# Optimization experiments

Hardware: AMD Instinct MI355X
Metric: run time of the kernel (lower is better)

The kernel has to match this reference:

```python
import jax, jax.numpy as jnp
import numpy as np

LAG = 5
MSG_HID = 256
N_ATOMS = 30
N_EDGES = N_ATOMS * (N_ATOMS - 1)  # 870
BATCH = 2
T = 200


def _rel_matrices():
    # fully-connected directed graph, no self loops (standard NRI encoding)
    recv, send = [], []
    for i in range(N_ATOMS):
        for j in range(N_ATOMS):
            if i != j:
                recv.append(i)
                send.append(j)
    rel_rec = np.zeros((N_EDGES, N_ATOMS), dtype=np.float32)
    rel_send = np.zeros((N_EDGES, N_ATOMS), dtype=np.float32)
    rel_rec[np.arange(N_EDGES), recv] = 1.0
    rel_send[np.arange(N_EDGES), send] = 1.0
    return jnp.asarray(rel_rec), jnp.asarray(rel_send)


def setup_inputs() -> dict:
    key = jax.random.key(0)
    ks = jax.random.split(key, 14)
    rel_rec, rel_send = _rel_matrices()
    s = 0.05
    return {
        "inputs": jax.random.normal(ks[0], (BATCH, N_ATOMS, T), jnp.float32),
        "mu": jax.random.normal(ks[1], (BATCH, N_EDGES), jnp.float32),
        "logvar": jax.random.normal(ks[2], (BATCH, N_EDGES), jnp.float32) * 0.1,
        "eps": jax.random.normal(ks[3], (BATCH, N_EDGES), jnp.float32),
        "rel_rec": rel_rec,
        "rel_send": rel_send,
        "w_msg1": jax.random.normal(ks[4], (2 * LAG, MSG_HID), jnp.float32) * s,
        "b_msg1": jnp.zeros((MSG_HID,), jnp.float32),
        "w_msg2": jax.random.normal(ks[5], (MSG_HID, MSG_HID), jnp.float32) * s,
        "b_msg2": jnp.zeros((MSG_HID,), jnp.float32),
        "w_out1": jax.random.normal(ks[6], (LAG + MSG_HID, MSG_HID), jnp.float32) * s,
        "b_out1": jnp.zeros((MSG_HID,), jnp.float32),
        "w_out2": jax.random.normal(ks[7], (MSG_HID, MSG_HID), jnp.float32) * s,
        "b_out2": jnp.zeros((MSG_HID,), jnp.float32),
        "w_out3": jax.random.normal(ks[8], (MSG_HID, 1), jnp.float32) * s,
        "b_out3": jnp.zeros((1,), jnp.float32),
    }


def reference(inputs, mu, logvar, eps, rel_rec, rel_send,
              w_msg1, b_msg1, w_msg2, b_msg2,
              w_out1, b_out1, w_out2, b_out2, w_out3, b_out3):
    # reparametrize: edges [B, E]
    edges = eps * jnp.exp(0.5 * logvar) + mu

    # lag-stack: data [B, T-lag, N, lag]
    Tm = inputs.shape[2] - LAG
    data = jnp.stack([inputs[:, :, i:i + Tm] for i in range(LAG)], axis=-1)
    data = jnp.transpose(data, (0, 2, 1, 3))  # [B, Tm, N, lag]

    # gather node features to edges via one-hot matmuls
    receivers = jnp.einsum('en,btnl->btel', rel_rec, data)   # [B, Tm, E, lag]
    senders = jnp.einsum('en,btnl->btel', rel_send, data)    # [B, Tm, E, lag]
    pre_msg = jnp.concatenate([senders, receivers], axis=-1)  # [B, Tm, E, 2*lag]

    msg = jax.nn.relu(pre_msg @ w_msg1 + b_msg1)
    msg = jax.nn.relu(msg @ w_msg2 + b_msg2)                 # [B, Tm, E, hid]
    msg = msg * edges[:, None, :, None]                       # edge mask

    # scatter-aggregate messages back to receiver nodes
    agg_msgs = jnp.einsum('bteh,en->btnh', msg, rel_rec)      # [B, Tm, N, hid]

    aug = jnp.concatenate([data, agg_msgs], axis=-1)          # [B, Tm, N, lag+hid]
    pred = jax.nn.relu(aug @ w_out1 + b_out1)
    pred = jax.nn.relu(pred @ w_out2 + b_out2)
    pred = (pred @ w_out3 + b_out3)[..., 0]                   # [B, Tm, N]

    return jnp.transpose(pred, (0, 2, 1))                     # [B, N, Tm]
```

## Files before the change

kernel.cpp:

```cpp
#include <hip/hip_runtime.h>

#define LAG 5
#define HID 256
#define NA 30
#define NE 870
#define TM 195
#define TT 200
#define NB 2
#define EPN 29
#define TB3 65
#define NROWS (NB * TM * NA)
#define APAD 4
#define KC 32
#define UVB 1463
#define W2F_ELEMS (HID * HID)
#define W1F_ELEMS (HID * 288)

typedef _Float16 f16;
typedef _Float16 f16x8 __attribute__((ext_vector_type(8)));
typedef float floatx4 __attribute__((ext_vector_type(4)));
typedef float floatx16 __attribute__((ext_vector_type(16)));

__global__ __launch_bounds__(256) void k1_prep(
    const float* __restrict__ inputs, const float* __restrict__ w_msg1,
    const float* __restrict__ b_msg1, const float* __restrict__ w_msg2,
    const float* __restrict__ w_out1, const float* __restrict__ w_out2,
    f16* __restrict__ u, f16* __restrict__ v, f16* __restrict__ w2frag,
    f16* __restrict__ w1frag, f16* __restrict__ w2ofrag)
{
    const int bid = blockIdx.x, tid = threadIdx.x;
    if (bid < UVB) {
        __shared__ float feats8[8][LAG];
        const int r0 = bid * 8;
        if (tid < 8 * LAG) {
            const int i = tid / LAG, l = tid % LAG;
            const int r = r0 + i;
            float fv = 0.f;
            if (r < NROWS) {
                const int b = r / (TM * NA), rem = r % (TM * NA);
                const int t = rem / NA, n = rem % NA;
                fv = inputs[(b * NA + n) * TT + t + l];
            }
            feats8[i][l] = fv;
        }
        float w1c[2 * LAG];
        #pragma unroll
        for (int k = 0; k < 2 * LAG; ++k) w1c[k] = w_msg1[k * HID + tid];
        const float bb = b_msg1[tid];
        __syncthreads();
        #pragma unroll
        for (int i = 0; i < 8; ++i) {
            const int r = r0 + i;
            if (r < NROWS) {
                float ua = bb, va = 0.f;
                #pragma unroll
                for (int l = 0; l < LAG; ++l) {
                    ua = fmaf(feats8[i][l], w1c[l], ua);
                    va = fmaf(feats8[i][l], w1c[LAG + l], va);
                }
                u[(r << 8) + tid] = (f16)ua;
                v[(r << 8) + tid] = (f16)va;
            }
        }
    } else if (bid < UVB + 32) {
        const int fidx = (bid - UVB) * 256 + tid;
        const int lane = fidx & 63;
        const int kc = (fidx >> 6) & 15;
        const int c32 = fidx >> 10;
        const int col = c32 * 32 + (lane & 31);
        const int kb = kc * 16 + (lane >> 5) * 8;
        f16x8 vv;
        #pragma unroll
        for (int x = 0; x < 8; ++x) vv[x] = (f16)w_msg2[(kb + x) * HID + col];
        *(f16x8*)&w2frag[fidx * 8] = vv;
    } else if (bid < UVB + 32 + 36) {
        const int fidx = (bid - (UVB + 32)) * 256 + tid;
        const int lane = fidx & 63;
        const int kc = (fidx >> 6) % 9;
        const int ntc = fidx / (64 * 9);
        const int col = ntc * 16 + (lane & 15);
        const int kb = kc * KC + (lane >> 4) * 8;
        f16x8 vv;
        #pragma unroll
        for (int x = 0; x < 8; ++x) {
            const int k = kb + x;
            float val;
            if (k < 256)      val = w_out1[(5 + k) * HID + col];
            else if (k < 261) val = w_out1[(k - 256) * HID + col];
            else              val = 0.f;
            vv[x] = (f16)val;
        }
        *(f16x8*)&w1frag[fidx * 8] = vv;
    } else {
        const int fidx = (bid - (UVB + 32 + 36)) * 256 + tid;
        const int lane = fidx & 63;
        const int kc = (fidx >> 6) & 7;
        const int ntc = fidx >> 9;
        const int col = ntc * 16 + (lane & 15);
        const int kb = kc * KC + (lane >> 4) * 8;
        f16x8 vv;
        #pragma unroll
        for (int x = 0; x < 8; ++x) vv[x] = (f16)w_out2[(kb + x) * HID + col];
        *(f16x8*)&w2ofrag[fidx * 8] = vv;
    }
}

__global__ __launch_bounds__(256, 3) void k2_msg(
    const f16* __restrict__ u, const f16* __restrict__ v,
    const f16* __restrict__ w2frag,
    const float* __restrict__ mu, const float* __restrict__ logvar,
    const float* __restrict__ eps, const float* __restrict__ b_msg2,
    f16* __restrict__ agg)
{
    __shared__ f16 a_lds[96 * 256];
    __shared__ float ev_lds[32];

    const int bid = blockIdx.x;
    const int n  = bid % NA;
    const int tb = (bid / NA) % TB3;
    const int b  = bid / (NA * TB3);
    const int t0 = tb * 3;
    const int tid = threadIdx.x;
    const int lane = tid & 63, w = tid >> 6;
    const int h = lane >> 5, l31 = lane & 31;

    if (tid < 32) {
        float evv = 0.f;
        if (tid < EPN) {
            const int e = b * NE + n * EPN + tid;
            evv = eps[e] * __expf(0.5f * logvar[e]) + mu[e];
        }
        ev_lds[tid] = evv;
    }

    const f16x8 z8 = {(f16)0, (f16)0, (f16)0, (f16)0, (f16)0, (f16)0, (f16)0, (f16)0};

    const int sbase = (b * TM + t0) * NA;
    #pragma unroll
    for (int i = 0; i < 12; ++i) {
        const int task = i * 256 + tid;
        const int row = task >> 5, c = task & 31;
        const int tt = row >> 5, ei = row & 31;
        f16x8 out8 = z8;
        if (ei < EPN) {
            const int j = ei + (ei >= n);
            const f16x8 uu = *(const f16x8*)(u + (((sbase + tt * NA + j) << 8) + c * 8));
            const f16x8 vv = *(const f16x8*)(v + (((sbase + tt * NA + n) << 8) + c * 8));
            out8 = __builtin_elementwise_max(uu + vv, z8);
        }
        *(f16x8*)&a_lds[row * 256 + ((c * 8) ^ ((row & 7) << 3))] = out8;
    }

    const f16* bbase = w2frag + (lane << 3);
    f16x8 b0[2], b1[2], b2[2];
    #pragma unroll
    for (int nt = 0; nt < 2; ++nt) {
        const int c32 = w * 2 + nt;
        b0[nt] = *(const f16x8*)(bbase + (((c32 * 16) + 0) << 9));
        b1[nt] = *(const f16x8*)(bbase + (((c32 * 16) + 1) << 9));
    }

    floatx16 acc[3][2];
    #pragma unroll
    for (int mt = 0; mt < 3; ++mt)
        #pragma unroll
        for (int nt = 0; nt < 2; ++nt)
            #pragma unroll
            for (int x = 0; x < 16; ++x) acc[mt][nt][x] = 0.f;

    __syncthreads();

    #pragma unroll
    for (int kc = 0; kc < 16; ++kc) {
        if (kc < 14) {
            #pragma unroll
            for (int nt = 0; nt < 2; ++nt)
                b2[nt] = *(const f16x8*)(bbase + ((((w * 2 + nt) * 16) + kc + 2) << 9));
        }
        f16x8 af[3];
        #pragma unroll
        for (int mt = 0; mt < 3; ++mt) {
            const int row = mt * 32 + l31;
            af[mt] = *(const f16x8*)&a_lds[row * 256 + ((kc * 16 + h * 8) ^ ((row & 7) << 3))];
        }
        #pragma unroll
        for (int nt = 0; nt < 2; ++nt)
            #pragma unroll
            for (int mt = 0; mt < 3; ++mt)
                acc[mt][nt] = __builtin_amdgcn_mfma_f32_32x32x16_f16(af[mt], b0[nt], acc[mt][nt], 0, 0, 0);
        #pragma unroll
        for (int nt = 0; nt < 2; ++nt) { b0[nt] = b1[nt]; b1[nt] = b2[nt]; }
    }

    float evr[16];
    #pragma unroll
    for (int reg = 0; reg < 16; ++reg)
        evr[reg] = ev_lds[(reg & 3) + 8 * (reg >> 2) + 4 * h];
    float b2s[2];
    #pragma unroll
    for (int nt = 0; nt < 2; ++nt) b2s[nt] = b_msg2[w * 64 + nt * 32 + l31];

    #pragma unroll
    for (int mt = 0; mt < 3; ++mt) {
        const int t = t0 + mt;
        #pragma unroll
        for (int nt = 0; nt < 2; ++nt) {
            float part = 0.f;
            #pragma unroll
            for (int reg = 0; reg < 16; ++reg)
                part += evr[reg] * fmaxf(acc[mt][nt][reg] + b2s[nt], 0.f);
            part += __shfl_xor(part, 32, 64);
            if (h == 0)
                agg[(((b * TM + t) * NA + n) << 8) + w * 64 + nt * 32 + l31] = (f16)part;
        }
    }
}

__global__ __launch_bounds__(256) void k3_out(
    const f16* __restrict__ agg, const float* __restrict__ inputs,
    const f16* __restrict__ w1frag, const f16* __restrict__ w2ofrag,
    const float* __restrict__ b_out1, const float* __restrict__ b_out2,
    const float* __restrict__ w_out3, const float* __restrict__ b_out3,
    float* __restrict__ out)
{
    __shared__ f16 a1[16][288 + APAD];
    __shared__ float red[4][16];

    const int R0 = blockIdx.x * 16;
    const int tid = threadIdx.x;
    const int lane = tid & 63, w = tid >> 6;
    const int q = lane >> 4, m15 = lane & 15;
    const int wbase = w * 64;

    #pragma unroll
    for (int i = 0; i < 2; ++i) {
        const int task = i * 256 + tid;
        const int row = task >> 5, c = task & 31;
        const int R = R0 + row;
        f16x8 val;
        if (R < NROWS) {
            val = *(const f16x8*)&agg[(R << 8) + c * 8];
        } else {
            for (int x = 0; x < 8; ++x) val[x] = (f16)0.f;
        }
        *(f16x8*)&a1[row][c * 8] = val;
    }
    if (tid < 16) {
        const int R = R0 + tid;
        if (R < NROWS) {
            const int b = R / (TM * NA), rem = R % (TM * NA);
            const int t = rem / NA, n = rem % NA;
            const float* ip = inputs + (b * NA + n) * TT + t;
            #pragma unroll
            for (int l = 0; l < LAG; ++l) a1[tid][256 + l] = (f16)ip[l];
            #pragma unroll
            for (int k = 261; k < 288; ++k) a1[tid][k] = (f16)0.f;
        } else {
            for (int k = 256; k < 288; ++k) a1[tid][k] = (f16)0.f;
        }
    }

    floatx4 acc[4];
    #pragma unroll
    for (int nt = 0; nt < 4; ++nt) acc[nt] = (floatx4){0.f, 0.f, 0.f, 0.f};

    const f16* b1base = w1frag + (lane << 3);
    f16x8 bcur[4], bnxt[4];
    #pragma unroll
    for (int nt = 0; nt < 4; ++nt)
        bcur[nt] = *(const f16x8*)(b1base + (((w * 4 + nt) * 9 + 0) << 9));

    __syncthreads();

    #pragma unroll
    for (int kc = 0; kc < 9; ++kc) {
        if (kc < 8) {
            #pragma unroll
            for (int nt = 0; nt < 4; ++nt)
                bnxt[nt] = *(const f16x8*)(b1base + (((w * 4 + nt) * 9 + kc + 1) << 9));
        }
        const f16x8 af = *(const f16x8*)&a1[m15][kc * KC + q * 8];
        #pragma unroll
        for (int nt = 0; nt < 4; ++nt)
            acc[nt] = __builtin_amdgcn_mfma_f32_16x16x32_f16(af, bcur[nt], acc[nt], 0, 0, 0);
        #pragma unroll
        for (int nt = 0; nt < 4; ++nt) bcur[nt] = bnxt[nt];
    }
    __syncthreads();

    {
        float b1v[4];
        #pragma unroll
        for (int nt = 0; nt < 4; ++nt) b1v[nt] = b_out1[wbase + nt * 16 + m15];
        #pragma unroll
        for (int nt = 0; nt < 4; ++nt)
            #pragma unroll
            for (int reg = 0; reg < 4; ++reg)
                a1[q * 4 + reg][wbase + nt * 16 + m15] =
                    (f16)fmaxf(acc[nt][reg] + b1v[nt], 0.f);
    }

    #pragma unroll
    for (int nt = 0; nt < 4; ++nt) acc[nt] = (floatx4){0.f, 0.f, 0.f, 0.f};

    const f16* b2base = w2ofrag + (lane << 3);
    #pragma unroll
    for (int nt = 0; nt < 4; ++nt)
        bcur[nt] = *(const f16x8*)(b2base + (((w * 4 + nt) * 8 + 0) << 9));

    __syncthreads();

    #pragma unroll
    for (int kc = 0; kc < 8; ++kc) {
        if (kc < 7) {
            #pragma unroll
            for (int nt = 0; nt < 4; ++nt)
                bnxt[nt] = *(const f16x8*)(b2base + (((w * 4 + nt) * 8 + kc + 1) << 9));
        }
        const f16x8 af = *(const f16x8*)&a1[m15][kc * KC + q * 8];
        #pragma unroll
        for (int nt = 0; nt < 4; ++nt)
            acc[nt] = __builtin_amdgcn_mfma_f32_16x16x32_f16(af, bcur[nt], acc[nt], 0, 0, 0);
        #pragma unroll
        for (int nt = 0; nt < 4; ++nt) bcur[nt] = bnxt[nt];
    }

    {
        float b2v[4], w3v[4];
        #pragma unroll
        for (int nt = 0; nt < 4; ++nt) {
            const int col = wbase + nt * 16 + m15;
            b2v[nt] = b_out2[col];
            w3v[nt] = w_out3[col];
        }
        #pragma unroll
        for (int reg = 0; reg < 4; ++reg) {
            float p = 0.f;
            #pragma unroll
            for (int nt = 0; nt < 4; ++nt)
                p += fmaxf(acc[nt][reg] + b2v[nt], 0.f) * w3v[nt];
            p += __shfl_xor(p, 1, 64);
            p += __shfl_xor(p, 2, 64);
            p += __shfl_xor(p, 4, 64);
            p += __shfl_xor(p, 8, 64);
            if (m15 == 0) red[w][q * 4 + reg] = p;
        }
    }
    __syncthreads();
    if (tid < 16) {
        const int R = R0 + tid;
        if (R < NROWS) {
            const float val = red[0][tid] + red[1][tid] + red[2][tid] + red[3][tid] + b_out3[0];
            const int b = R / (TM * NA), rem = R % (TM * NA);
            const int t = rem / NA, n = rem % NA;
            out[(b * NA + n) * TM + t] = val;
        }
    }
}

extern "C" void kernel_launch(void* const* d_in, const int* in_sizes, int n_in,
                              void* d_out, int out_size, void* d_ws, size_t ws_size,
                              hipStream_t stream) {
    const float* inputs  = (const float*)d_in[0];
    const float* mu      = (const float*)d_in[1];
    const float* logvar  = (const float*)d_in[2];
    const float* eps     = (const float*)d_in[3];
    const float* w_msg1  = (const float*)d_in[6];
    const float* b_msg1  = (const float*)d_in[7];
    const float* w_msg2  = (const float*)d_in[8];
    const float* b_msg2  = (const float*)d_in[9];
    const float* w_out1  = (const float*)d_in[10];
    const float* b_out1  = (const float*)d_in[11];
    const float* w_out2  = (const float*)d_in[12];
    const float* b_out2  = (const float*)d_in[13];
    const float* w_out3  = (const float*)d_in[14];
    const float* b_out3  = (const float*)d_in[15];
    float* out = (float*)d_out;

    f16* u       = (f16*)d_ws;
    f16* v       = u       + NROWS * HID;
    f16* aggw    = v       + NROWS * HID;
    f16* w2frag  = aggw    + NROWS * HID;
    f16* w1frag  = w2frag  + W2F_ELEMS;
    f16* w2ofrag = w1frag  + W1F_ELEMS;

    hipLaunchKernelGGL(k1_prep, dim3(UVB + 32 + 36 + 32), dim3(256), 0, stream,
                       inputs, w_msg1, b_msg1, w_msg2, w_out1, w_out2,
                       u, v, w2frag, w1frag, w2ofrag);
    hipLaunchKernelGGL(k2_msg, dim3(NB * NA * TB3), dim3(256), 0, stream,
                       u, v, w2frag, mu, logvar, eps, b_msg2, aggw);
    hipLaunchKernelGGL(k3_out, dim3((NROWS + 15) / 16), dim3(256), 0, stream,
                       aggw, inputs, w1frag, w2ofrag, b_out1, b_out2, w_out3, b_out3, out);
}
```

Measured before the change: 162.8 us.

## Use 8-wave k2 blocks, XCD-aware block remap, and MFMA priority hints

```diff
diff --git a/kernel.cpp b/kernel.cpp
--- a/kernel.cpp
+++ b/kernel.cpp
@@ -15,6 +15,9 @@
 #define UVB 1463
 #define W2F_ELEMS (HID * HID)
 #define W1F_ELEMS (HID * 288)
+#define NWG2 (NB * NA * TB3)
+#define Q8 (NWG2 / 8)
+#define R8 (NWG2 % 8)
 
 typedef _Float16 f16;
 typedef _Float16 f16x8 __attribute__((ext_vector_type(8)));
@@ -105,7 +108,7 @@
     }
 }
 
-__global__ __launch_bounds__(256, 3) void k2_msg(
+__global__ __launch_bounds__(512, 4) void k2_msg(
     const f16* __restrict__ u, const f16* __restrict__ v,
     const f16* __restrict__ w2frag,
     const float* __restrict__ mu, const float* __restrict__ logvar,
@@ -115,7 +118,10 @@
     __shared__ f16 a_lds[96 * 256];
     __shared__ float ev_lds[32];
 
-    const int bid = blockIdx.x;
+    const int bid0 = blockIdx.x;
+    const int xcd = bid0 & 7, sub = bid0 >> 3;
+    const int bid = (xcd < R8 ? xcd * (Q8 + 1) : R8 * (Q8 + 1) + (xcd - R8) * Q8) + sub;
+
     const int n  = bid % NA;
     const int tb = (bid / NA) % TB3;
     const int b  = bid / (NA * TB3);
@@ -137,8 +143,8 @@
 
     const int sbase = (b * TM + t0) * NA;
     #pragma unroll
-    for (int i = 0; i < 12; ++i) {
-        const int task = i * 256 + tid;
+    for (int i = 0; i < 6; ++i) {
+        const int task = i * 512 + tid;
         const int row = task >> 5, c = task & 31;
         const int tt = row >> 5, ei = row & 31;
         f16x8 out8 = z8;
@@ -151,68 +157,52 @@
         *(f16x8*)&a_lds[row * 256 + ((c * 8) ^ ((row & 7) << 3))] = out8;
     }
 
-    const f16* bbase = w2frag + (lane << 3);
-    f16x8 b0[2], b1[2], b2[2];
-    #pragma unroll
-    for (int nt = 0; nt < 2; ++nt) {
-        const int c32 = w * 2 + nt;
-        b0[nt] = *(const f16x8*)(bbase + (((c32 * 16) + 0) << 9));
-        b1[nt] = *(const f16x8*)(bbase + (((c32 * 16) + 1) << 9));
-    }
-
-    floatx16 acc[3][2];
+    const f16* bbase = w2frag + ((w * 16) << 9) + (lane << 3);
+    f16x8 b0 = *(const f16x8*)(bbase + (0 << 9));
+    f16x8 b1 = *(const f16x8*)(bbase + (1 << 9));
+
+    floatx16 acc[3];
     #pragma unroll
     for (int mt = 0; mt < 3; ++mt)
         #pragma unroll
-        for (int nt = 0; nt < 2; ++nt)
-            #pragma unroll
-            for (int x = 0; x < 16; ++x) acc[mt][nt][x] = 0.f;
+        for (int x = 0; x < 16; ++x) acc[mt][x] = 0.f;
 
     __syncthreads();
 
     #pragma unroll
     for (int kc = 0; kc < 16; ++kc) {
-        if (kc < 14) {
-            #pragma unroll
-            for (int nt = 0; nt < 2; ++nt)
-                b2[nt] = *(const f16x8*)(bbase + ((((w * 2 + nt) * 16) + kc + 2) << 9));
-        }
+        f16x8 b2 = b1;
+        if (kc < 14) b2 = *(const f16x8*)(bbase + ((kc + 2) << 9));
         f16x8 af[3];
         #pragma unroll
         for (int mt = 0; mt < 3; ++mt) {
             const int row = mt * 32 + l31;
             af[mt] = *(const f16x8*)&a_lds[row * 256 + ((kc * 16 + h * 8) ^ ((row & 7) << 3))];
         }
-        #pragma unroll
-        for (int nt = 0; nt < 2; ++nt)
-            #pragma unroll
-            for (int mt = 0; mt < 3; ++mt)
-                acc[mt][nt] = __builtin_amdgcn_mfma_f32_32x32x16_f16(af[mt], b0[nt], acc[mt][nt], 0, 0, 0);
-        #pragma unroll
-        for (int nt = 0; nt < 2; ++nt) { b0[nt] = b1[nt]; b1[nt] = b2[nt]; }
+        __builtin_amdgcn_s_setprio(1);
+        #pragma unroll
+        for (int mt = 0; mt < 3; ++mt)
+            acc[mt] = __builtin_amdgcn_mfma_f32_32x32x16_f16(af[mt], b0, acc[mt], 0, 0, 0);
+        __builtin_amdgcn_s_setprio(0);
+        b0 = b1; b1 = b2;
     }
 
     float evr[16];
     #pragma unroll
     for (int reg = 0; reg < 16; ++reg)
         evr[reg] = ev_lds[(reg & 3) + 8 * (reg >> 2) + 4 * h];
-    float b2s[2];
-    #pragma unroll
-    for (int nt = 0; nt < 2; ++nt) b2s[nt] = b_msg2[w * 64 + nt * 32 + l31];
+    const float b2s = b_msg2[w * 32 + l31];
 
     #pragma unroll
     for (int mt = 0; mt < 3; ++mt) {
         const int t = t0 + mt;
-        #pragma unroll
-        for (int nt = 0; nt < 2; ++nt) {
-            float part = 0.f;
-            #pragma unroll
-            for (int reg = 0; reg < 16; ++reg)
-                part += evr[reg] * fmaxf(acc[mt][nt][reg] + b2s[nt], 0.f);
-            part += __shfl_xor(part, 32, 64);
-            if (h == 0)
-                agg[(((b * TM + t) * NA + n) << 8) + w * 64 + nt * 32 + l31] = (f16)part;
-        }
+        float part = 0.f;
+        #pragma unroll
+        for (int reg = 0; reg < 16; ++reg)
+            part += evr[reg] * fmaxf(acc[mt][reg] + b2s, 0.f);
+        part += __shfl_xor(part, 32, 64);
+        if (h == 0)
+            agg[(((b * TM + t) * NA + n) << 8) + w * 32 + l31] = (f16)part;
     }
 }
 
@@ -387,7 +377,7 @@
     hipLaunchKernelGGL(k1_prep, dim3(UVB + 32 + 36 + 32), dim3(256), 0, stream,
                        inputs, w_msg1, b_msg1, w_msg2, w_out1, w_out2,
                        u, v, w2frag, w1frag, w2ofrag);
-    hipLaunchKernelGGL(k2_msg, dim3(NB * NA * TB3), dim3(256), 0, stream,
+    hipLaunchKernelGGL(k2_msg, dim3(NWG2), dim3(512), 0, stream,
                        u, v, w2frag, mu, logvar, eps, b_msg2, aggw);
     hipLaunchKernelGGL(k3_out, dim3((NROWS + 15) / 16), dim3(256), 0, stream,
                        aggw, inputs, w1frag, w2ofrag, b_out1, b_out2, w_out3, b_out3, out);
```

Result: no change. 165.1 us (+1.4%).
